# Optimization experiments

Hardware: AMD Instinct MI355X
Metric: run time of the kernel (lower is better)

Reference implementation:

```python
import jax, jax.numpy as jnp
import numpy as np

B, S, H = 16, 4096, 1024

def setup_inputs() -> dict:
    key = jax.random.key(0)
    k1, k2, k3, k4, k5 = jax.random.split(key, 5)
    x = jax.random.normal(k1, (B, S, H), dtype=jnp.float32)
    lengths = jax.random.randint(k2, (B,), 1, S + 1, dtype=jnp.int32)
    W = jax.random.normal(k3, (H, H), dtype=jnp.float32) * (1.0 / np.sqrt(H))
    b = jax.random.normal(k4, (H,), dtype=jnp.float32) * 0.01
    key_vec = jax.random.normal(k5, (H,), dtype=jnp.float32)
    return {"x": x, "lengths": lengths, "W": W, "b": b, "key_vec": key_vec}

def reference(x, lengths, W, b, key_vec):
    # query = tanh(Linear(x)) : [B,S,H]
    query = jnp.tanh(jnp.einsum('bsh,oh->bso', x, W) + b)
    # scores = query @ key_vec : [B,S]
    scores = jnp.einsum('bsh,h->bs', query, key_vec)
    # masked softmax over valid positions (equivalent to per-sample slice softmax)
    seq_len = x.shape[1]
    valid = jnp.arange(seq_len)[None, :] < lengths[:, None]  # [B,S]
    scores = jnp.where(valid, scores, -jnp.inf)
    attn = jax.nn.softmax(scores, axis=-1)  # masked positions get 0
    # weighted sum of x : [B,H]
    return jnp.einsum('bs,bsh->bh', attn, x)
```

## Files before the change

kernel.cpp:

```cpp
#include <hip/hip_runtime.h>
#include <math.h>

#define BB 16
#define SS 4096
#define HH 1024
#define SCH 64


typedef __attribute__((ext_vector_type(8))) short bf16x8;
typedef __attribute__((ext_vector_type(16))) float f32x16;

__device__ __forceinline__ void gl_lds16(const void* g, void* l) {
  __builtin_amdgcn_global_load_lds(
      (const __attribute__((address_space(1))) void*)g,
      (__attribute__((address_space(3))) void*)l, 16, 0, 0);
}

__global__ __launch_bounds__(256) void conv_w(const float* __restrict__ W,
                                              unsigned short* __restrict__ Bbuf) {
  int ct = blockIdx.x, kc = blockIdx.y;
  unsigned short* blk = Bbuf + (size_t)(ct * 32 + kc) * 8192;
  int tid = threadIdx.x;
#pragma unroll
  for (int it = 0; it < 16; ++it) {
    int flat = it * 256 + tid;
    int n = flat >> 5, kk = flat & 31;
    float f = W[(size_t)(ct * 128 + n) * HH + kc * 32 + kk];
    unsigned u = __float_as_uint(f);
    float hf = __uint_as_float(u & 0xffff0000u);
    int slot = (kk >> 3) ^ ((n >> 1) & 3);
    int idx = n * 32 + slot * 8 + (kk & 7);
    blk[idx] = (unsigned short)(u >> 16);
    blk[4096 + idx] = (unsigned short)(__float_as_uint(f - hf) >> 16);
  }
}

__global__ __launch_bounds__(256, 2) void scores_gemm(
    const float* __restrict__ x, const int* __restrict__ lengths,
    const unsigned short* __restrict__ Bbuf, const float* __restrict__ bias,
    const float* __restrict__ key, float* __restrict__ scores) {
  int f = blockIdx.y * 8 + blockIdx.x;
  int r8 = f & 7, j = f >> 3;
  int t = r8 + (j & ~7);
  int ct = j & 7;
  int b = t >> 5;
  int s0 = (t & 31) * 128;
  if (s0 >= lengths[b]) return;

  __shared__ char lds[65536];
  char* A0 = lds;
  char* B0 = lds + 16384;
  char* A1 = lds + 32768;
  char* B1 = lds + 49152;

  int tid = threadIdx.x;
  int lane = tid & 63, w = tid >> 6;
  int wm = w & 1, wn = w >> 1;

  f32x16 acc[2][2];
#pragma unroll
  for (int mt = 0; mt < 2; ++mt)
#pragma unroll
    for (int nt = 0; nt < 2; ++nt)
#pragma unroll
      for (int i = 0; i < 16; ++i) acc[mt][nt][i] = 0.f;

  const float* xb = x + ((size_t)b * SS + s0) * HH;
  const char* Bblk0 = (const char*)Bbuf + (size_t)ct * 32 * 16384;

  int ar = tid >> 3;
  int ak8 = tid & 7;
  int awoff = (((ak8 >> 1) ^ ((ar >> 1) & 3)) << 4) + ((ak8 & 1) << 3);

  int mrow = lane & 31;
  int khsel = lane >> 5;
  int rx = (mrow >> 1) & 3;
  int soff0 = ((khsel ^ rx)) << 4;
  int soff1 = (((2 + khsel) ^ rx)) << 4;
  int rbA = (wm * 64 + mrow) * 64;
  int rbB = (wn * 64 + mrow) * 64;

  float4 v[4];

#define STAGE_ISSUE(KC, BDST)                                              \
  {                                                                        \
    const char* Bblk = Bblk0 + (KC) * 16384;                               \
    _Pragma("unroll") for (int i = 0; i < 4; ++i) {                        \
      int c = w * 4 + i;                                                   \
      gl_lds16(Bblk + c * 1024 + lane * 16, (BDST) + c * 1024);            \
    }                                                                      \
    _Pragma("unroll") for (int it = 0; it < 4; ++it)                       \
      v[it] = *(const float4*)(xb + (size_t)(ar + it * 32) * HH +          \
                               (KC) * 32 + ak8 * 4);                       \
  }

#define A_WRITE(ADST)                                                      \
  {                                                                        \
    _Pragma("unroll") for (int it = 0; it < 4; ++it) {                     \
      int rr = ar + it * 32;                                               \
      unsigned u0 = __float_as_uint(v[it].x), u1 = __float_as_uint(v[it].y);\
      unsigned u2 = __float_as_uint(v[it].z), u3 = __float_as_uint(v[it].w);\
      float l0 = v[it].x - __uint_as_float(u0 & 0xffff0000u);              \
      float l1 = v[it].y - __uint_as_float(u1 & 0xffff0000u);              \
      float l2 = v[it].z - __uint_as_float(u2 & 0xffff0000u);              \
      float l3 = v[it].w - __uint_as_float(u3 & 0xffff0000u);              \
      uint2 hp, lp;                                                        \
      hp.x = (u0 >> 16) | (u1 & 0xffff0000u);                              \
      hp.y = (u2 >> 16) | (u3 & 0xffff0000u);                              \
      lp.x = (__float_as_uint(l0) >> 16) | (__float_as_uint(l1) & 0xffff0000u);\
      lp.y = (__float_as_uint(l2) >> 16) | (__float_as_uint(l3) & 0xffff0000u);\
      *(uint2*)((ADST) + rr * 64 + awoff) = hp;                            \
      *(uint2*)((ADST) + 8192 + rr * 64 + awoff) = lp;                     \
    }                                                                      \
  }

#define COMPUTE(AC, BC)                                                    \
  {                                                                        \
    _Pragma("unroll") for (int kh = 0; kh < 2; ++kh) {                     \
      int so = kh ? soff1 : soff0;                                         \
      bf16x8 ah[2], al[2], bh[2], bl[2];                                   \
      _Pragma("unroll") for (int mt = 0; mt < 2; ++mt) {                   \
        ah[mt] = *(bf16x8*)((AC) + rbA + mt * 2048 + so);                  \
        al[mt] = *(bf16x8*)((AC) + 8192 + rbA + mt * 2048 + so);           \
        bh[mt] = *(bf16x8*)((BC) + rbB + mt * 2048 + so);                  \
        bl[mt] = *(bf16x8*)((BC) + 8192 + rbB + mt * 2048 + so);           \
      }                                                                    \
      _Pragma("unroll") for (int mt = 0; mt < 2; ++mt)                     \
        _Pragma("unroll") for (int nt = 0; nt < 2; ++nt) {                 \
          acc[mt][nt] = __builtin_amdgcn_mfma_f32_32x32x16_bf16(           \
              ah[mt], bh[nt], acc[mt][nt], 0, 0, 0);                       \
          acc[mt][nt] = __builtin_amdgcn_mfma_f32_32x32x16_bf16(           \
              ah[mt], bl[nt], acc[mt][nt], 0, 0, 0);                       \
          acc[mt][nt] = __builtin_amdgcn_mfma_f32_32x32x16_bf16(           \
              al[mt], bh[nt], acc[mt][nt], 0, 0, 0);                       \
        }                                                                  \
    }                                                                      \
  }

  STAGE_ISSUE(0, B0)
  A_WRITE(A0)
  __syncthreads();

  for (int kc = 0; kc < 32; kc += 2) {
    STAGE_ISSUE(kc + 1, B1)
    COMPUTE(A0, B0)
    A_WRITE(A1)
    __syncthreads();
    if (kc + 2 < 32) { STAGE_ISSUE(kc + 2, B0) }
    COMPUTE(A1, B1)
    if (kc + 2 < 32) { A_WRITE(A0) }
    __syncthreads();
  }

#undef STAGE_ISSUE
#undef A_WRITE
#undef COMPUTE

  int col = lane & 31;
  int rbase = (lane >> 5) * 4;
  float bo[2], ko[2];
#pragma unroll
  for (int nt = 0; nt < 2; ++nt) {
    int o = ct * 128 + wn * 64 + nt * 32 + col;
    bo[nt] = bias[o];
    ko[nt] = key[o];
  }
  float* srow = scores + (size_t)b * SS + s0;
#pragma unroll
  for (int mt = 0; mt < 2; ++mt) {
#pragma unroll
    for (int reg = 0; reg < 16; ++reg) {
      float sv = tanhf(acc[mt][0][reg] + bo[0]) * ko[0] +
                 tanhf(acc[mt][1][reg] + bo[1]) * ko[1];
#pragma unroll
      for (int off = 1; off < 32; off <<= 1) sv += __shfl_xor(sv, off);
      if (col == 0) {
        int row = wm * 64 + mt * 32 + (reg & 3) + 8 * (reg >> 2) + rbase;
        atomicAdd(srow + row, sv);
      }
    }
  }
}

__global__ __launch_bounds__(1024) void softmax_kernel(float* __restrict__ sc,
                                                       const int* __restrict__ lengths) {
  int b = blockIdx.x;
  int L = lengths[b];
  float* p = sc + (size_t)b * SS;
  __shared__ float sred[18];
  int tid = threadIdx.x;

  float m = -3.0e38f;
  for (int s = tid; s < L; s += 1024) m = fmaxf(m, p[s]);
  for (int off = 32; off > 0; off >>= 1) m = fmaxf(m, __shfl_down(m, off));
  if ((tid & 63) == 0) sred[tid >> 6] = m;
  __syncthreads();
  if (tid == 0) {
    float mm = sred[0];
    for (int w = 1; w < 16; ++w) mm = fmaxf(mm, sred[w]);
    sred[16] = mm;
  }
  __syncthreads();
  m = sred[16];

  float z = 0.f;
  for (int s = tid; s < L; s += 1024) {
    float e = expf(p[s] - m);
    p[s] = e;
    z += e;
  }
  for (int off = 32; off > 0; off >>= 1) z += __shfl_down(z, off);
  if ((tid & 63) == 0) sred[tid >> 6] = z;
  __syncthreads();
  if (tid == 0) {
    float zz = 0.f;
    for (int w = 0; w < 16; ++w) zz += sred[w];
    sred[17] = zz;
  }
  __syncthreads();
  float inv = 1.f / sred[17];
  for (int s = tid; s < L; s += 1024) p[s] *= inv;
}

__global__ __launch_bounds__(256) void wsum_partial(const float* __restrict__ x,
                                                    const float* __restrict__ p,
                                                    const int* __restrict__ lengths,
                                                    float* __restrict__ part) {
  int b = blockIdx.y;
  int L = lengths[b];
  int c = blockIdx.x;
  int sbeg = c * SCH;
  if (sbeg >= L) return;
  int send = min(sbeg + SCH, L);
  int h = threadIdx.x * 4;
  const float* xb = x + (size_t)b * SS * HH + h;
  const float* pb = p + (size_t)b * SS;
  float4 acc = {0.f, 0.f, 0.f, 0.f};
  int s = sbeg;
  for (; s + 8 <= send; s += 8) {
    float4 pa = *(const float4*)(pb + s);
    float4 pc = *(const float4*)(pb + s + 4);
    float4 vv[8];
#pragma unroll
    for (int jj = 0; jj < 8; ++jj)
      vv[jj] = *(const float4*)(xb + (size_t)(s + jj) * HH);
    float pw[8] = {pa.x, pa.y, pa.z, pa.w, pc.x, pc.y, pc.z, pc.w};
#pragma unroll
    for (int jj = 0; jj < 8; ++jj) {
      acc.x = fmaf(pw[jj], vv[jj].x, acc.x);
      acc.y = fmaf(pw[jj], vv[jj].y, acc.y);
      acc.z = fmaf(pw[jj], vv[jj].z, acc.z);
      acc.w = fmaf(pw[jj], vv[jj].w, acc.w);
    }
  }
  for (; s < send; ++s) {
    float wgt = pb[s];
    float4 vx = *(const float4*)(xb + (size_t)s * HH);
    acc.x = fmaf(wgt, vx.x, acc.x);
    acc.y = fmaf(wgt, vx.y, acc.y);
    acc.z = fmaf(wgt, vx.z, acc.z);
    acc.w = fmaf(wgt, vx.w, acc.w);
  }
  *(float4*)(part + ((size_t)b * (SS / SCH) + c) * HH + h) = acc;
}

__global__ __launch_bounds__(256) void wsum_reduce(const float* __restrict__ part,
                                                   const int* __restrict__ lengths,
                                                   float* __restrict__ out) {
  int b = blockIdx.x;
  int nc = (lengths[b] + SCH - 1) / SCH;
  int h = threadIdx.x * 4;
  const float* pb = part + (size_t)b * (SS / SCH) * HH + h;
  float4 acc = {0.f, 0.f, 0.f, 0.f};
  int c = 0;
  for (; c + 8 <= nc; c += 8) {
    float4 v[8];
#pragma unroll
    for (int j = 0; j < 8; ++j) v[j] = *(const float4*)(pb + (size_t)(c + j) * HH);
#pragma unroll
    for (int j = 0; j < 8; ++j) {
      acc.x += v[j].x; acc.y += v[j].y; acc.z += v[j].z; acc.w += v[j].w;
    }
  }
  for (; c < nc; ++c) {
    float4 v = *(const float4*)(pb + (size_t)c * HH);
    acc.x += v.x; acc.y += v.y; acc.z += v.z; acc.w += v.w;
  }
  *(float4*)(out + (size_t)b * HH + h) = acc;
}

extern "C" void kernel_launch(void* const* d_in, const int* in_sizes, int n_in,
                              void* d_out, int out_size, void* d_ws, size_t ws_size,
                              hipStream_t stream) {
  const float* x = (const float*)d_in[0];
  const int* lengths = (const int*)d_in[1];
  const float* W = (const float*)d_in[2];
  const float* bias = (const float*)d_in[3];
  const float* key = (const float*)d_in[4];
  float* out = (float*)d_out;

  unsigned short* Bbuf = (unsigned short*)d_ws;
  float* part = (float*)d_ws;
  float* scores = (float*)((char*)d_ws + (size_t)4 * 1024 * 1024);

  hipMemsetAsync(scores, 0, (size_t)BB * SS * sizeof(float), stream);
  conv_w<<<dim3(8, 32), 256, 0, stream>>>(W, Bbuf);
  scores_gemm<<<dim3(8, 512), 256, 0, stream>>>(x, lengths, Bbuf, bias, key, scores);
  softmax_kernel<<<dim3(BB), 1024, 0, stream>>>(scores, lengths);
  wsum_partial<<<dim3(SS / SCH, BB), 256, 0, stream>>>(x, scores, lengths, part);
  wsum_reduce<<<dim3(BB), 256, 0, stream>>>(part, lengths, out);
}
```

Measured before the change: 580.8 us.

## Fuse tile-local softmax and weighted sum into GEMM epilogue via last-block counter

The last of the 8 column blocks for each 128-row tile, detected with an atomic counter, computes a local max, exp-sum and exp-weighted sum of x for its rows. These partials are then merged by a small online-softmax combine kernel. This removes the separate softmax, partial-sum and reduce kernels, and the second full-grid pass over x, while the x tile is probably still in cache. The cost is serialized work at the tail of some blocks and reliance on atomic visibility and fences across blocks.

```diff
diff --git a/kernel.cpp b/kernel.cpp
--- a/kernel.cpp
+++ b/kernel.cpp
@@ -38,7 +38,9 @@
 __global__ __launch_bounds__(256, 2) void scores_gemm(
     const float* __restrict__ x, const int* __restrict__ lengths,
     const unsigned short* __restrict__ Bbuf, const float* __restrict__ bias,
-    const float* __restrict__ key, float* __restrict__ scores) {
+    const float* __restrict__ key, float* __restrict__ scores,
+    int* __restrict__ cnt, float* __restrict__ mzb, float* __restrict__ vb,
+    int fused) {
   int f = blockIdx.y * 8 + blockIdx.x;
   int r8 = f & 7, j = f >> 3;
   int t = r8 + (j & ~7);
@@ -180,6 +182,100 @@
       }
     }
   }
+
+  if (!fused) return;
+
+  __threadfence();
+  __syncthreads();
+  float* fl = (float*)lds;
+  float* sc_l = fl;
+  float* e_l = fl + 128;
+  float* red = fl + 256;
+  int* flagI = (int*)(fl + 280);
+  if (tid == 0) flagI[0] = (atomicAdd(&cnt[t], 1) == 7) ? 1 : 0;
+  __syncthreads();
+  if (!flagI[0]) return;
+
+  int L = lengths[b];
+  int rv = min(128, L - s0);
+
+  if (tid < 128) {
+    float s = (tid < rv) ? atomicAdd(&srow[tid], 0.0f) : 0.f;
+    sc_l[tid] = s;
+  }
+  __syncthreads();
+
+  if (tid < 128) {
+    float mv = (tid < rv) ? sc_l[tid] : -3.0e38f;
+#pragma unroll
+    for (int off = 32; off > 0; off >>= 1) mv = fmaxf(mv, __shfl_xor(mv, off));
+    if ((tid & 63) == 0) red[tid >> 6] = mv;
+  }
+  __syncthreads();
+  float m_t = fmaxf(red[0], red[1]);
+
+  if (tid < 128) {
+    float e = (tid < rv) ? expf(sc_l[tid] - m_t) : 0.f;
+    e_l[tid] = e;
+#pragma unroll
+    for (int off = 32; off > 0; off >>= 1) e += __shfl_xor(e, off);
+    if ((tid & 63) == 0) red[2 + (tid >> 6)] = e;
+  }
+  __syncthreads();
+  float z_t = red[2] + red[3];
+
+  int h4 = tid << 2;
+  float4 a4 = {0.f, 0.f, 0.f, 0.f};
+  int r = 0;
+  for (; r + 8 <= rv; r += 8) {
+    float4 xv[8];
+#pragma unroll
+    for (int jj = 0; jj < 8; ++jj)
+      xv[jj] = *(const float4*)(xb + (size_t)(r + jj) * HH + h4);
+#pragma unroll
+    for (int jj = 0; jj < 8; ++jj) {
+      float ww = e_l[r + jj];
+      a4.x = fmaf(ww, xv[jj].x, a4.x);
+      a4.y = fmaf(ww, xv[jj].y, a4.y);
+      a4.z = fmaf(ww, xv[jj].z, a4.z);
+      a4.w = fmaf(ww, xv[jj].w, a4.w);
+    }
+  }
+  for (; r < rv; ++r) {
+    float ww = e_l[r];
+    float4 xv = *(const float4*)(xb + (size_t)r * HH + h4);
+    a4.x = fmaf(ww, xv.x, a4.x);
+    a4.y = fmaf(ww, xv.y, a4.y);
+    a4.z = fmaf(ww, xv.z, a4.z);
+    a4.w = fmaf(ww, xv.w, a4.w);
+  }
+  *(float4*)(vb + (size_t)t * HH + h4) = a4;
+  if (tid == 0) { mzb[2 * t] = m_t; mzb[2 * t + 1] = z_t; }
+}
+
+__global__ __launch_bounds__(256) void combine_kernel(
+    const float* __restrict__ mzb, const float* __restrict__ vb,
+    const int* __restrict__ lengths, float* __restrict__ out) {
+  int b = blockIdx.x;
+  int L = lengths[b];
+  int nt = (L + 127) >> 7;
+  float M = -3.0e38f;
+  for (int tt = 0; tt < nt; ++tt) M = fmaxf(M, mzb[2 * (b * 32 + tt)]);
+  float Z = 0.f;
+  for (int tt = 0; tt < nt; ++tt)
+    Z += mzb[2 * (b * 32 + tt) + 1] * expf(mzb[2 * (b * 32 + tt)] - M);
+  float inv = 1.f / Z;
+  int h4 = threadIdx.x << 2;
+  float4 a4 = {0.f, 0.f, 0.f, 0.f};
+  for (int tt = 0; tt < nt; ++tt) {
+    float wv = expf(mzb[2 * (b * 32 + tt)] - M) * inv;
+    float4 v4 = *(const float4*)(vb + (size_t)(b * 32 + tt) * HH + h4);
+    a4.x = fmaf(wv, v4.x, a4.x);
+    a4.y = fmaf(wv, v4.y, a4.y);
+    a4.z = fmaf(wv, v4.z, a4.z);
+    a4.w = fmaf(wv, v4.w, a4.w);
+  }
+  *(float4*)(out + (size_t)b * HH + h4) = a4;
 }
 
 __global__ __launch_bounds__(1024) void softmax_kernel(float* __restrict__ sc,
@@ -276,10 +372,10 @@
   for (; c + 8 <= nc; c += 8) {
     float4 v[8];
 #pragma unroll
-    for (int j = 0; j < 8; ++j) v[j] = *(const float4*)(pb + (size_t)(c + j) * HH);
-#pragma unroll
-    for (int j = 0; j < 8; ++j) {
-      acc.x += v[j].x; acc.y += v[j].y; acc.z += v[j].z; acc.w += v[j].w;
+    for (int jj = 0; jj < 8; ++jj) v[jj] = *(const float4*)(pb + (size_t)(c + jj) * HH);
+#pragma unroll
+    for (int jj = 0; jj < 8; ++jj) {
+      acc.x += v[jj].x; acc.y += v[jj].y; acc.z += v[jj].z; acc.w += v[jj].w;
     }
   }
   for (; c < nc; ++c) {
@@ -299,14 +395,29 @@
   const float* key = (const float*)d_in[4];
   float* out = (float*)d_out;
 
-  unsigned short* Bbuf = (unsigned short*)d_ws;
-  float* part = (float*)d_ws;
-  float* scores = (float*)((char*)d_ws + (size_t)4 * 1024 * 1024);
-
-  hipMemsetAsync(scores, 0, (size_t)BB * SS * sizeof(float), stream);
-  conv_w<<<dim3(8, 32), 256, 0, stream>>>(W, Bbuf);
-  scores_gemm<<<dim3(8, 512), 256, 0, stream>>>(x, lengths, Bbuf, bias, key, scores);
-  softmax_kernel<<<dim3(BB), 1024, 0, stream>>>(scores, lengths);
-  wsum_partial<<<dim3(SS / SCH, BB), 256, 0, stream>>>(x, scores, lengths, part);
-  wsum_reduce<<<dim3(BB), 256, 0, stream>>>(part, lengths, out);
-}
+  char* ws = (char*)d_ws;
+  unsigned short* Bbuf = (unsigned short*)ws;
+  float* scores = (float*)(ws + (size_t)4 * 1024 * 1024);
+  int* cnt = (int*)(ws + (size_t)4 * 1024 * 1024 + 256 * 1024);
+  float* mzb = (float*)(ws + (size_t)4 * 1024 * 1024 + 258 * 1024);
+  float* vbuf = (float*)(ws + (size_t)4 * 1024 * 1024 + 272 * 1024);
+  const size_t NEED = (size_t)4 * 1024 * 1024 + 272 * 1024 + (size_t)2 * 1024 * 1024;
+
+  if (ws_size >= NEED) {
+    hipMemsetAsync(scores, 0, 258 * 1024, stream);
+    conv_w<<<dim3(8, 32), 256, 0, stream>>>(W, Bbuf);
+    scores_gemm<<<dim3(8, 512), 256, 0, stream>>>(x, lengths, Bbuf, bias, key,
+                                                  scores, cnt, mzb, vbuf, 1);
+    combine_kernel<<<dim3(BB), 256, 0, stream>>>(mzb, vbuf, lengths, out);
+  } else {
+    float* part = (float*)ws;
+    hipMemsetAsync(scores, 0, (size_t)BB * SS * sizeof(float), stream);
+    conv_w<<<dim3(8, 32), 256, 0, stream>>>(W, Bbuf);
+    scores_gemm<<<dim3(8, 512), 256, 0, stream>>>(x, lengths, Bbuf, bias, key,
+                                                  scores, (int*)nullptr,
+                                                  (float*)nullptr, (float*)nullptr, 0);
+    softmax_kernel<<<dim3(BB), 1024, 0, stream>>>(scores, lengths);
+    wsum_partial<<<dim3(SS / SCH, BB), 256, 0, stream>>>(x, scores, lengths, part);
+    wsum_reduce<<<dim3(BB), 256, 0, stream>>>(part, lengths, out);
+  }
+}
```

After: 739.2 us. 1.27x slower.
